# Optimization experiments

Measured on AMD Instinct MI355X. Metric: run time of the kernel, lower is better.

Reference implementation:

```python
import jax, jax.numpy as jnp
import numpy as np

NUM_HEADS = 8
NUM_GROUPS = 32
EPS = 1e-5


def group_norm(x, scale, bias):
    # x: (b, c, t)
    b, c, t = x.shape
    xg = x.reshape(b, NUM_GROUPS, c // NUM_GROUPS, t)
    mean = xg.mean(axis=(2, 3), keepdims=True)
    var = xg.var(axis=(2, 3), keepdims=True)
    xn = ((xg - mean) * jax.lax.rsqrt(var + EPS)).reshape(b, c, t)
    return xn * scale[None, :, None] + bias[None, :, None]


def setup_inputs() -> dict:
    key = jax.random.key(0)
    ks = jax.random.split(key, 3)
    b, c, h, w = 16, 512, 32, 32
    x = jax.random.normal(ks[0], (b, c, h, w), dtype=jnp.float32)
    gn_scale = jnp.ones((c,), jnp.float32)
    gn_bias = jnp.zeros((c,), jnp.float32)
    w_qkv = jax.random.normal(ks[1], (3 * c, c), jnp.float32) * (c ** -0.5)
    b_qkv = jnp.zeros((3 * c,), jnp.float32)
    w_proj = jax.random.normal(ks[2], (c, c), jnp.float32) * (c ** -0.5)
    b_proj = jnp.zeros((c,), jnp.float32)
    return {"x": x, "gn_scale": gn_scale, "gn_bias": gn_bias,
            "w_qkv": w_qkv, "b_qkv": b_qkv, "w_proj": w_proj, "b_proj": b_proj}


def reference(x, gn_scale, gn_bias, w_qkv, b_qkv, w_proj, b_proj):
    b, c, h, w = x.shape
    t = h * w
    xf = x.reshape(b, c, t)
    xn = group_norm(xf, gn_scale, gn_bias)
    # 1x1 conv1d == channel matmul: (b, 3c, t)
    qkv = jnp.einsum('oc,bct->bot', w_qkv, xn) + b_qkv[None, :, None]
    dh = c // NUM_HEADS
    qkv = qkv.reshape(b * NUM_HEADS, 3 * dh, t)
    q, k, v = jnp.split(qkv, 3, axis=1)  # each (b*H, dh, t)
    scale = dh ** -0.25
    logits = jnp.einsum('bct,bcs->bts', q * scale, k * scale)
    weight = jax.nn.softmax(logits.astype(jnp.float32), axis=-1).astype(logits.dtype)
    attn = jnp.einsum('bts,bcs->bct', weight, v)  # (b*H, dh, t)
    attn = attn.reshape(b, c, t)
    out = jnp.einsum('oc,bct->bot', w_proj, attn) + b_proj[None, :, None]
    return (xf + out).reshape(b, c, h, w)
```

## Files before the change

kernel.cpp:

```cpp
#include <hip/hip_runtime.h>
#include <hip/hip_bf16.h>

typedef __hip_bfloat16 bf16;
typedef __attribute__((ext_vector_type(8))) short short8;
typedef __attribute__((ext_vector_type(4))) short short4v;
typedef __attribute__((ext_vector_type(4))) float float4v;
typedef __attribute__((ext_vector_type(16))) float f32x16;
typedef __attribute__((ext_vector_type(4))) int int4v;

__device__ __forceinline__ float b2f(bf16 v) { return __bfloat162float(v); }
__device__ __forceinline__ bf16  f2b(float v) { return __float2bfloat16(v); }
__device__ __forceinline__ short f2s(float v) { bf16 h = f2b(v); return *reinterpret_cast<short*>(&h); }
__device__ __forceinline__ float s2f(short s) { bf16 h; *reinterpret_cast<short*>(&h) = s; return b2f(h); }
__device__ __forceinline__ short8 ld8(const bf16* p) { return *(const short8*)p; }

__device__ __forceinline__ float ldin(const void* p, size_t i, int f32) {
  return f32 ? ((const float*)p)[i] : b2f(((const bf16*)p)[i]);
}

__device__ __forceinline__ float4v mfma16(short8 a, short8 b, float4v c) {
  return __builtin_amdgcn_mfma_f32_16x16x32_bf16(a, b, c, 0, 0, 0);
}
__device__ __forceinline__ f32x16 mfma32(short8 a, short8 b, f32x16 c) {
  return __builtin_amdgcn_mfma_f32_32x32x16_bf16(a, b, c, 0, 0, 0);
}
__device__ __forceinline__ int cvtpk(float a, float b) {
  int r; asm("v_cvt_pk_bf16_f32 %0, %1, %2" : "=v"(r) : "v"(a), "v"(b)); return r;
}
__device__ __forceinline__ void plswap(int& x, int& y) {
  asm("v_permlane32_swap_b32 %0, %1" : "+v"(x), "+v"(y));
}

__device__ __forceinline__ void gload16(const void* g, void* l) {
  __builtin_amdgcn_global_load_lds((__attribute__((address_space(1))) void*)(void*)g,
                                   (__attribute__((address_space(3))) void*)l, 16, 0, 0);
}

#define K2SCALE 0.18033688011112042f
#define TSTRIDE 72

__global__ __launch_bounds__(256) void detect_kernel(const unsigned short* __restrict__ x,
                                                     int* __restrict__ flag) {
  __shared__ int h;
  if (threadIdx.x == 0) h = 0;
  __syncthreads();
  int local = 0;
  for (int i = threadIdx.x; i < 8192; i += 256)
    if ((x[i] & 0x7F80u) == 0x7F80u) local = 1;
  if (local) atomicOr(&h, 1);
  __syncthreads();
  if (threadIdx.x == 0) *flag = h;
}

__global__ __launch_bounds__(256) void conv2_kernel(const void* __restrict__ s1, bf16* __restrict__ d1,
                                                    const void* __restrict__ s2, bf16* __restrict__ d2,
                                                    const void* __restrict__ s3, bf16* __restrict__ d3,
                                                    const void* __restrict__ s4, bf16* __restrict__ d4,
                                                    const int* __restrict__ flagp) {
  const int f32 = *flagp;
  const int blk = blockIdx.x;
  const void* src; bf16* dst; int base, n;
  if (blk < 768)       { src = s1; dst = d1; base = blk;        n = 786432; }
  else if (blk < 1024) { src = s2; dst = d2; base = blk - 768;  n = 262144; }
  else if (blk < 1026) { src = s3; dst = d3; base = blk - 1024; n = 1536;   }
  else                 { src = s4; dst = d4; base = 0;          n = 512;    }
  int i0 = (base * 256 + threadIdx.x) * 4;
#pragma unroll
  for (int j = 0; j < 4; j++) {
    int i = i0 + j;
    if (i < n) dst[i] = f2b(ldin(src, i, f32));
  }
}

__global__ __launch_bounds__(256) void gn_stats_kernel(const void* __restrict__ x,
                                                       float2* __restrict__ stats,
                                                       const int* __restrict__ flagp) {
  const int f32 = *flagp;
  const int bg = blockIdx.x;
  const int GSZ = 16 * 1024;
  const size_t base = (size_t)bg * GSZ;
  const int tid = threadIdx.x;

  float s = 0.f, ss = 0.f;
  if (f32) {
    const float4v* xp = (const float4v*)((const float*)x + base) + tid;
#pragma unroll
    for (int i = 0; i < 16; i++) {
      float4v v = xp[i * 256];
#pragma unroll
      for (int j = 0; j < 4; j++) { s += v[j]; ss += v[j] * v[j]; }
    }
  } else {
    const short8* xp = (const short8*)((const bf16*)x + base) + tid;
#pragma unroll
    for (int i = 0; i < 8; i++) {
      short8 v = xp[i * 256];
#pragma unroll
      for (int j = 0; j < 8; j++) { float f = s2f(v[j]); s += f; ss += f * f; }
    }
  }
  for (int off = 32; off > 0; off >>= 1) {
    s  += __shfl_down(s, off);
    ss += __shfl_down(ss, off);
  }
  __shared__ float rs[4], rss[4];
  const int wave = tid >> 6, lane = tid & 63;
  if (lane == 0) { rs[wave] = s; rss[wave] = ss; }
  __syncthreads();
  if (tid == 0) {
    s  = rs[0] + rs[1] + rs[2] + rs[3];
    ss = rss[0] + rss[1] + rss[2] + rss[3];
    const float mean = s * (1.f / GSZ);
    const float var  = ss * (1.f / GSZ) - mean * mean;
    stats[bg] = make_float2(mean, rsqrtf(var + 1e-5f));
  }
}

__global__ __launch_bounds__(256) void gn_apply_kernel(const void* __restrict__ x,
                                                       const void* __restrict__ gsc,
                                                       const void* __restrict__ gbi,
                                                       const float2* __restrict__ stats,
                                                       bf16* __restrict__ xn,
                                                       const int* __restrict__ flagp) {
  const int f32 = *flagp;
  const int b = blockIdx.y;
  const int t0 = blockIdx.x * 64;
  const int cs = blockIdx.z * 128;
  const int tid = threadIdx.x;

  __shared__ float Aa[128], Bb[128];
  __shared__ short T[64][130];

  if (tid < 128) {
    const int c = cs + tid;
    const float2 st = stats[b * 32 + (c >> 4)];
    const float sc = ldin(gsc, c, f32), bi = ldin(gbi, c, f32);
    Aa[tid] = st.y * sc;
    Bb[tid] = bi - st.x * st.y * sc;
  }
  __syncthreads();

  const int row = tid >> 4;
  const int t4 = (tid & 15) * 4;
  if (f32) {
    const float* xb = (const float*)x + ((size_t)(b * 512 + cs)) * 1024 + t0 + t4;
#pragma unroll
    for (int st = 0; st < 8; st++) {
      const int c = row + st * 16;
      const float4v v = *(const float4v*)(xb + (size_t)c * 1024);
      const float aa = Aa[c], bb = Bb[c];
#pragma unroll
      for (int j = 0; j < 4; j++) T[t4 + j][c] = f2s(v[j] * aa + bb);
    }
  } else {
    const bf16* xb = (const bf16*)x + ((size_t)(b * 512 + cs)) * 1024 + t0 + t4;
#pragma unroll
    for (int st = 0; st < 8; st++) {
      const int c = row + st * 16;
      const short4v v = *(const short4v*)(xb + (size_t)c * 1024);
      const float aa = Aa[c], bb = Bb[c];
#pragma unroll
      for (int j = 0; j < 4; j++) T[t4 + j][c] = f2s(s2f(v[j]) * aa + bb);
    }
  }
  __syncthreads();

  const int cc = (tid & 63) * 2, tr = tid >> 6;
#pragma unroll
  for (int i = 0; i < 16; i++) {
    const int t2 = tr + i * 4;
    const int v = *(const int*)&T[t2][cc];
    *(int*)&xn[((size_t)(b * 1024 + t0 + t2)) * 512 + cs + cc] = v;
  }
}

__global__ __launch_bounds__(256) void qkv_kernel(const bf16* __restrict__ Wb,
                                                  const bf16* __restrict__ biasb,
                                                  const bf16* __restrict__ xn,
                                                  bf16* __restrict__ Qt,
                                                  bf16* __restrict__ Kt,
                                                  bf16* __restrict__ Vb) {
  const int bat = blockIdx.z;
  const int M0 = blockIdx.y * 128;
  const int N0 = blockIdx.x * 128;
  __shared__ short smem[18432];

  const int tid = threadIdx.x;
  const int w = tid >> 6, lane = tid & 63;
  const int col = lane & 15, g = lane >> 4;
  const int wm = (w & 1) * 64, wn = (w >> 1) * 64;

  float4v acc[4][4];
#pragma unroll
  for (int i = 0; i < 4; i++)
#pragma unroll
    for (int j = 0; j < 4; j++) acc[i][j] = (float4v)(0.f);

  int srco[2], dstb[2];
#pragma unroll
  for (int i = 0; i < 2; i++) {
    const int Gb = i * 256 + w * 64;
    dstb[i] = Gb * 8;
    const int G = Gb + lane;
    srco[i] = (G >> 2) * 512 + (G & 3) * 8;
  }
  const bf16* Ab  = Wb + (size_t)M0 * 512;
  const bf16* Bb2 = xn + ((size_t)bat * 1024 + N0) * 512;

#pragma unroll
  for (int i = 0; i < 2; i++) {
    gload16(Ab + srco[i],  &smem[dstb[i]]);
    gload16(Bb2 + srco[i], &smem[4096 + dstb[i]]);
  }
  __syncthreads();

  for (int it = 0; it < 16; ++it) {
    const int pb = it & 1;
    if (it < 15) {
      const int kn = it * 32 + 32;
      const int nb = (1 - pb) * 8192;
#pragma unroll
      for (int i = 0; i < 2; i++) {
        gload16(Ab + kn + srco[i],  &smem[nb + dstb[i]]);
        gload16(Bb2 + kn + srco[i], &smem[nb + 4096 + dstb[i]]);
      }
    }
    const short* Ap = &smem[pb * 8192];
    const short* Bp = Ap + 4096;
    short8 af[4], bf4[4];
#pragma unroll
    for (int mt = 0; mt < 4; mt++) af[mt] = *(const short8*)&Ap[(wm + mt * 16 + col) * 32 + g * 8];
#pragma unroll
    for (int nt = 0; nt < 4; nt++) bf4[nt] = *(const short8*)&Bp[(wn + nt * 16 + col) * 32 + g * 8];
#pragma unroll
    for (int mt = 0; mt < 4; mt++)
#pragma unroll
      for (int nt = 0; nt < 4; nt++) acc[mt][nt] = mfma16(af[mt], bf4[nt], acc[mt][nt]);
    __syncthreads();
  }

  const int sec = (M0 + wm) >> 6;
  const int h = sec / 3, kind = sec % 3;
  const size_t bh = (size_t)bat * 8 + h;
  const float qs = (kind == 0) ? K2SCALE : 1.f;
  short* Tw = smem + w * 4608;

  float bv[4][4];
#pragma unroll
  for (int mt = 0; mt < 4; mt++)
#pragma unroll
    for (int r = 0; r < 4; r++) bv[mt][r] = b2f(biasb[M0 + wm + mt * 16 + g * 4 + r]);

  if (kind == 2) {
#pragma unroll
    for (int mt = 0; mt < 4; mt++)
#pragma unroll
      for (int nt = 0; nt < 4; nt++)
#pragma unroll
        for (int r = 0; r < 4; r++) {
          const int lo = mt * 16 + g * 4 + r;
          const int lt = nt * 16 + col;
          Tw[lo * TSTRIDE + lt] = f2s(acc[mt][nt][r] + bv[mt][r]);
        }
#pragma unroll
    for (int j = 0; j < 8; j++) {
      const int lo = j * 8 + (lane >> 3);
      const int gr = lane & 7;
      short8 v = *(const short8*)&Tw[lo * TSTRIDE + gr * 8];
      *(short8*)(Vb + (bh * 64 + lo) * 1024 + N0 + wn + gr * 8) = v;
    }
  } else {
#pragma unroll
    for (int mt = 0; mt < 4; mt++)
#pragma unroll
      for (int nt = 0; nt < 4; nt++) {
        short4v pk;
#pragma unroll
        for (int r = 0; r < 4; r++) pk[r] = f2s((acc[mt][nt][r] + bv[mt][r]) * qs);
        *(short4v*)&Tw[(nt * 16 + col) * TSTRIDE + mt * 16 + g * 4] = pk;
      }
    bf16* dst = (kind == 0) ? Qt : Kt;
#pragma unroll
    for (int j = 0; j < 8; j++) {
      const int tl = j * 8 + (lane >> 3), c8 = (lane & 7) * 8;
      short8 v = *(const short8*)&Tw[tl * TSTRIDE + c8];
      *(short8*)(dst + (bh * 1024 + N0 + wn + tl) * 64 + c8) = v;
    }
  }
}

__global__ __launch_bounds__(256, 2) void attn_kernel(const bf16* __restrict__ Qt,
                                                      const bf16* __restrict__ Kt,
                                                      const bf16* __restrict__ Vb,
                                                      bf16* __restrict__ xattn) {
  const int bh = blockIdx.x;
  const int t0 = blockIdx.y * 256;
  const int b = bh >> 3, h = bh & 7;
  const int tid = threadIdx.x;
  const int w = tid >> 6, lane = tid & 63;
  const int qv = lane & 31, hh = lane >> 5;
  const int q0 = t0 + w * 64;

  __shared__ short Ks[8192];
  __shared__ short Vs[8192];

  const bf16* kbase = Kt + (size_t)bh * 65536;
  const bf16* vbase = Vb + (size_t)bh * 65536;

  int ksrc[2], vsrc[2];
  const int ldst0 = w * 1024, ldst1 = w * 1024 + 512;
#pragma unroll
  for (int i = 0; i < 2; i++) {
    const int G = w * 128 + i * 64 + lane;
    const int a = G >> 8, ks = (G >> 6) & 3, qvs = (G >> 1) & 31, hhs = G & 1;
    const int co = (ks * 2 + hhs) * 8;
    ksrc[i] = (a * 32 + qvs) * 64 + co;
    vsrc[i] = (a * 32 + qvs) * 1024 + co;
  }
  const int rb = (qv * 2 + hh) * 8;

  short8 qb[2][4];
#pragma unroll
  for (int qt = 0; qt < 2; qt++)
#pragma unroll
    for (int ks = 0; ks < 4; ks++)
      qb[qt][ks] = ld8(Qt + ((size_t)bh * 1024 + q0 + qt * 32 + qv) * 64 + ks * 16 + hh * 8);

  f32x16 O[2][2];
#pragma unroll
  for (int qt = 0; qt < 2; qt++)
#pragma unroll
    for (int o = 0; o < 2; o++) O[qt][o] = (f32x16)(0.f);
  float l[2] = {0.f, 0.f};
  short8 pa[2][4];

  gload16(kbase + ksrc[0], &Ks[ldst0]);
  gload16(kbase + ksrc[1], &Ks[ldst1]);
  gload16(vbase + vsrc[0], &Vs[ldst0]);
  gload16(vbase + vsrc[1], &Vs[ldst1]);
  __syncthreads();

#define SMAX(S, qt, a)                                                          \
  {                                                                             \
    _Pragma("unroll")                                                           \
    for (int j = 0; j < 16; j++) S[j] = __builtin_amdgcn_exp2f(S[j]);           \
    l[qt] += (((S[0] + S[1]) + (S[2] + S[3])) + ((S[4] + S[5]) + (S[6] + S[7])))\
       + (((S[8] + S[9]) + (S[10] + S[11])) + ((S[12] + S[13]) + (S[14] + S[15]))); \
    _Pragma("unroll")                                                           \
    for (int kp = 0; kp < 2; kp++) {                                            \
      int X  = cvtpk(S[8 * kp + 0], S[8 * kp + 1]);                             \
      int Y  = cvtpk(S[8 * kp + 4], S[8 * kp + 5]);                             \
      int X2 = cvtpk(S[8 * kp + 2], S[8 * kp + 3]);                             \
      int Y2 = cvtpk(S[8 * kp + 6], S[8 * kp + 7]);                             \
      plswap(X, Y);                                                             \
      plswap(X2, Y2);                                                           \
      const int4v wv = {X, X2, Y, Y2};                                          \
      pa[qt][(a) * 2 + kp] = __builtin_bit_cast(short8, wv);                    \
    }                                                                           \
  }

#pragma unroll 2
  for (int it = 0; it < 16; ++it) {
    const int cur = (it & 1) * 4096;
    const int nxt = 4096 - cur;
    if (it < 15) {
      gload16(kbase + (it + 1) * 4096 + ksrc[0], &Ks[nxt + ldst0]);
      gload16(kbase + (it + 1) * 4096 + ksrc[1], &Ks[nxt + ldst1]);
      gload16(vbase + (it + 1) * 64 + vsrc[0],   &Vs[nxt + ldst0]);
      gload16(vbase + (it + 1) * 64 + vsrc[1],   &Vs[nxt + ldst1]);
    }
#pragma unroll
    for (int a = 0; a < 2; a++) {
      short8 kf[4];
#pragma unroll
      for (int ks = 0; ks < 4; ks++)
        kf[ks] = *(const short8*)&Ks[cur + (a * 4 + ks) * 512 + rb];
#pragma unroll
      for (int qt = 0; qt < 2; qt++) {
        f32x16 S = (f32x16)(0.f);
#pragma unroll
        for (int ks = 0; ks < 4; ks++) S = mfma32(kf[ks], qb[qt][ks], S);
        SMAX(S, qt, a);
      }
    }
#pragma unroll
    for (int o = 0; o < 2; o++) {
      short8 vf[4];
#pragma unroll
      for (int ks = 0; ks < 4; ks++)
        vf[ks] = *(const short8*)&Vs[cur + (o * 4 + ks) * 512 + rb];
#pragma unroll
      for (int qt = 0; qt < 2; qt++)
#pragma unroll
        for (int ks = 0; ks < 4; ks++)
          O[qt][o] = mfma32(pa[qt][ks], vf[ks], O[qt][o]);
    }
    __syncthreads();
  }
#undef SMAX

#pragma unroll
  for (int qt = 0; qt < 2; qt++) {
    float lt = l[qt] + __shfl_xor(l[qt], 32);
    const float inv = 1.f / lt;
    float* lf = (float*)Ks + w * 64 + qt * 32;
    lf[qv] = inv;

    bf16* ob = xattn + ((size_t)b * 1024 + q0 + qt * 32 + 4 * hh) * 512 + h * 64 + qv;
#pragma unroll
    for (int r = 0; r < 16; r++) {
      const int qoff = (r & 3) + 8 * (r >> 2);
      const float iv = lf[qoff + 4 * hh];
      ob[(size_t)qoff * 512]      = f2b(O[qt][0][r] * iv);
      ob[(size_t)qoff * 512 + 32] = f2b(O[qt][1][r] * iv);
    }
  }
}

__global__ __launch_bounds__(256) void proj_kernel(const bf16* __restrict__ Wp,
                                                   const bf16* __restrict__ biasb,
                                                   const bf16* __restrict__ xattn,
                                                   const void* __restrict__ res,
                                                   void* __restrict__ out,
                                                   const int* __restrict__ flagp) {
  const int f32 = *flagp;
  const int bat = blockIdx.z;
  const int M0 = blockIdx.y * 128;
  const int N0 = blockIdx.x * 128;
  __shared__ short smem[18432];

  const int tid = threadIdx.x;
  const int w = tid >> 6, lane = tid & 63;
  const int col = lane & 15, g = lane >> 4;
  const int wm = (w & 1) * 64, wn = (w >> 1) * 64;

  float4v acc[4][4];
#pragma unroll
  for (int i = 0; i < 4; i++)
#pragma unroll
    for (int j = 0; j < 4; j++) acc[i][j] = (float4v)(0.f);

  int srco[2], dstb[2];
#pragma unroll
  for (int i = 0; i < 2; i++) {
    const int Gb = i * 256 + w * 64;
    dstb[i] = Gb * 8;
    const int G = Gb + lane;
    srco[i] = (G >> 2) * 512 + (G & 3) * 8;
  }
  const bf16* Ab  = Wp + (size_t)M0 * 512;
  const bf16* Bb2 = xattn + ((size_t)bat * 1024 + N0) * 512;

#pragma unroll
  for (int i = 0; i < 2; i++) {
    gload16(Ab + srco[i],  &smem[dstb[i]]);
    gload16(Bb2 + srco[i], &smem[4096 + dstb[i]]);
  }
  __syncthreads();

  for (int it = 0; it < 16; ++it) {
    const int pb = it & 1;
    if (it < 15) {
      const int kn = it * 32 + 32;
      const int nb = (1 - pb) * 8192;
#pragma unroll
      for (int i = 0; i < 2; i++) {
        gload16(Ab + kn + srco[i],  &smem[nb + dstb[i]]);
        gload16(Bb2 + kn + srco[i], &smem[nb + 4096 + dstb[i]]);
      }
    }
    const short* Ap = &smem[pb * 8192];
    const short* Bp = Ap + 4096;
    short8 af[4], bf4[4];
#pragma unroll
    for (int mt = 0; mt < 4; mt++) af[mt] = *(const short8*)&Ap[(wm + mt * 16 + col) * 32 + g * 8];
#pragma unroll
    for (int nt = 0; nt < 4; nt++) bf4[nt] = *(const short8*)&Bp[(wn + nt * 16 + col) * 32 + g * 8];
#pragma unroll
    for (int mt = 0; mt < 4; mt++)
#pragma unroll
      for (int nt = 0; nt < 4; nt++) acc[mt][nt] = mfma16(af[mt], bf4[nt], acc[mt][nt]);
    __syncthreads();
  }

  short* Tw = smem + w * 4608;
  float bv[4][4];
#pragma unroll
  for (int mt = 0; mt < 4; mt++)
#pragma unroll
    for (int r = 0; r < 4; r++) bv[mt][r] = b2f(biasb[M0 + wm + mt * 16 + g * 4 + r]);

#pragma unroll
  for (int mt = 0; mt < 4; mt++)
#pragma unroll
    for (int nt = 0; nt < 4; nt++)
#pragma unroll
      for (int r = 0; r < 4; r++) {
        const int lo = mt * 16 + g * 4 + r;
        const int lt = nt * 16 + col;
        Tw[lo * TSTRIDE + lt] = f2s(acc[mt][nt][r] + bv[mt][r]);
      }
#pragma unroll
  for (int j = 0; j < 8; j++) {
    const int lo = j * 8 + (lane >> 3);
    const int gr = lane & 7;
    short8 v = *(const short8*)&Tw[lo * TSTRIDE + gr * 8];
    const int o = M0 + wm + lo;
    const size_t ci = ((size_t)bat * 512 + o) * 1024 + N0 + wn + gr * 8;
    if (f32) {
      float4v o0, o1;
#pragma unroll
      for (int e = 0; e < 4; e++) o0[e] = s2f(v[e]) + ((const float*)res)[ci + e];
#pragma unroll
      for (int e = 0; e < 4; e++) o1[e] = s2f(v[e + 4]) + ((const float*)res)[ci + 4 + e];
      *(float4v*)((float*)out + ci) = o0;
      *(float4v*)((float*)out + ci + 4) = o1;
    } else {
      short8 ov;
#pragma unroll
      for (int e = 0; e < 8; e++)
        ov[e] = f2s(s2f(v[e]) + b2f(((const bf16*)res)[ci + e]));
      *(short8*)((bf16*)out + ci) = ov;
    }
  }
}

extern "C" void kernel_launch(void* const* d_in, const int* in_sizes, int n_in,
                              void* d_out, int out_size, void* d_ws, size_t ws_size,
                              hipStream_t stream) {
  const void* x      = d_in[0];
  const void* gsc    = d_in[1];
  const void* gbi    = d_in[2];
  const void* w_qkv  = d_in[3];
  const void* b_qkv  = d_in[4];
  const void* w_proj = d_in[5];
  const void* b_proj = d_in[6];

  char* p = (char*)d_ws;
  int*    flag  = (int*)p;                 p += 256;
  float2* stats = (float2*)p;              p += 512 * sizeof(float2);
  bf16*   xn    = (bf16*)p;                p += (size_t)16 * 1024 * 512 * 2;
  bf16*   Qt    = (bf16*)p;                p += (size_t)128 * 1024 * 64 * 2;
  bf16*   Kt    = (bf16*)p;                p += (size_t)128 * 1024 * 64 * 2;
  bf16*   Vb    = (bf16*)p;                p += (size_t)128 * 64 * 1024 * 2;
  bf16*   Wqb   = (bf16*)p;                p += (size_t)1536 * 512 * 2;
  bf16*   Wpb   = (bf16*)p;                p += (size_t)512 * 512 * 2;
  bf16*   Bqb   = (bf16*)p;                p += (size_t)1536 * 2;
  bf16*   Bpb   = (bf16*)p;                p += (size_t)512 * 2;
  bf16*   xattn = (bf16*)p;

  detect_kernel<<<1, 256, 0, stream>>>((const unsigned short*)x, flag);
  conv2_kernel<<<1027, 256, 0, stream>>>(w_qkv, Wqb, w_proj, Wpb,
                                         b_qkv, Bqb, b_proj, Bpb, flag);
  gn_stats_kernel<<<512, 256, 0, stream>>>(x, stats, flag);
  gn_apply_kernel<<<dim3(16, 16, 4), 256, 0, stream>>>(x, gsc, gbi, stats, xn, flag);
  qkv_kernel<<<dim3(8, 12, 16), 256, 0, stream>>>(Wqb, Bqb, xn, Qt, Kt, Vb);
  attn_kernel<<<dim3(128, 4), 256, 0, stream>>>(Qt, Kt, Vb, xattn);
  proj_kernel<<<dim3(8, 4, 16), 256, 0, stream>>>(Wpb, Bpb, xattn, x, d_out, flag);
}
```

Before: 206.2 us.

## Halve queries per attention block, double grid, raise occupancy and MFMA priority

Each attention wave now handles 32 queries instead of 64, so every block covers 128 queries and the grid doubles to 1024 blocks. Launch bounds rise to 4 blocks per CU, which cuts register use per thread and should let more waves hide latency. s_setprio is raised around the MFMA sequences so matrix work is issued ahead of other waves. The cost is that each K/V tile loaded into shared memory is reused by half as many queries, doubling total K/V traffic.

```diff
diff --git a/kernel.cpp b/kernel.cpp
--- a/kernel.cpp
+++ b/kernel.cpp
@@ -289,17 +289,17 @@
   }
 }
 
-__global__ __launch_bounds__(256, 2) void attn_kernel(const bf16* __restrict__ Qt,
+__global__ __launch_bounds__(256, 4) void attn_kernel(const bf16* __restrict__ Qt,
                                                       const bf16* __restrict__ Kt,
                                                       const bf16* __restrict__ Vb,
                                                       bf16* __restrict__ xattn) {
   const int bh = blockIdx.x;
-  const int t0 = blockIdx.y * 256;
+  const int t0 = blockIdx.y * 128;
   const int b = bh >> 3, h = bh & 7;
   const int tid = threadIdx.x;
   const int w = tid >> 6, lane = tid & 63;
   const int qv = lane & 31, hh = lane >> 5;
-  const int q0 = t0 + w * 64;
+  const int q0 = t0 + w * 32;
 
   __shared__ short Ks[8192];
   __shared__ short Vs[8192];
@@ -319,20 +319,15 @@
   }
   const int rb = (qv * 2 + hh) * 8;
 
-  short8 qb[2][4];
-#pragma unroll
-  for (int qt = 0; qt < 2; qt++)
-#pragma unroll
-    for (int ks = 0; ks < 4; ks++)
-      qb[qt][ks] = ld8(Qt + ((size_t)bh * 1024 + q0 + qt * 32 + qv) * 64 + ks * 16 + hh * 8);
-
-  f32x16 O[2][2];
-#pragma unroll
-  for (int qt = 0; qt < 2; qt++)
-#pragma unroll
-    for (int o = 0; o < 2; o++) O[qt][o] = (f32x16)(0.f);
-  float l[2] = {0.f, 0.f};
-  short8 pa[2][4];
+  short8 qb[4];
+#pragma unroll
+  for (int ks = 0; ks < 4; ks++)
+    qb[ks] = ld8(Qt + ((size_t)bh * 1024 + q0 + qv) * 64 + ks * 16 + hh * 8);
+
+  f32x16 O[2];
+  O[0] = (f32x16)(0.f); O[1] = (f32x16)(0.f);
+  float l = 0.f;
+  short8 pa[4];
 
   gload16(kbase + ksrc[0], &Ks[ldst0]);
   gload16(kbase + ksrc[1], &Ks[ldst1]);
@@ -340,11 +335,11 @@
   gload16(vbase + vsrc[1], &Vs[ldst1]);
   __syncthreads();
 
-#define SMAX(S, qt, a)                                                          \
+#define SMAX(S, a)                                                              \
   {                                                                             \
     _Pragma("unroll")                                                           \
     for (int j = 0; j < 16; j++) S[j] = __builtin_amdgcn_exp2f(S[j]);           \
-    l[qt] += (((S[0] + S[1]) + (S[2] + S[3])) + ((S[4] + S[5]) + (S[6] + S[7])))\
+    l += (((S[0] + S[1]) + (S[2] + S[3])) + ((S[4] + S[5]) + (S[6] + S[7])))    \
        + (((S[8] + S[9]) + (S[10] + S[11])) + ((S[12] + S[13]) + (S[14] + S[15]))); \
     _Pragma("unroll")                                                           \
     for (int kp = 0; kp < 2; kp++) {                                            \
@@ -355,7 +350,7 @@
       plswap(X, Y);                                                             \
       plswap(X2, Y2);                                                           \
       const int4v wv = {X, X2, Y, Y2};                                          \
-      pa[qt][(a) * 2 + kp] = __builtin_bit_cast(short8, wv);                    \
+      pa[(a) * 2 + kp] = __builtin_bit_cast(short8, wv);                        \
     }                                                                           \
   }
 
@@ -375,13 +370,12 @@
 #pragma unroll
       for (int ks = 0; ks < 4; ks++)
         kf[ks] = *(const short8*)&Ks[cur + (a * 4 + ks) * 512 + rb];
-#pragma unroll
-      for (int qt = 0; qt < 2; qt++) {
-        f32x16 S = (f32x16)(0.f);
-#pragma unroll
-        for (int ks = 0; ks < 4; ks++) S = mfma32(kf[ks], qb[qt][ks], S);
-        SMAX(S, qt, a);
-      }
+      f32x16 S = (f32x16)(0.f);
+      __builtin_amdgcn_s_setprio(1);
+#pragma unroll
+      for (int ks = 0; ks < 4; ks++) S = mfma32(kf[ks], qb[ks], S);
+      __builtin_amdgcn_s_setprio(0);
+      SMAX(S, a);
     }
 #pragma unroll
     for (int o = 0; o < 2; o++) {
@@ -389,30 +383,29 @@
 #pragma unroll
       for (int ks = 0; ks < 4; ks++)
         vf[ks] = *(const short8*)&Vs[cur + (o * 4 + ks) * 512 + rb];
-#pragma unroll
-      for (int qt = 0; qt < 2; qt++)
-#pragma unroll
-        for (int ks = 0; ks < 4; ks++)
-          O[qt][o] = mfma32(pa[qt][ks], vf[ks], O[qt][o]);
+      __builtin_amdgcn_s_setprio(1);
+#pragma unroll
+      for (int ks = 0; ks < 4; ks++)
+        O[o] = mfma32(pa[ks], vf[ks], O[o]);
+      __builtin_amdgcn_s_setprio(0);
     }
     __syncthreads();
   }
 #undef SMAX
 
-#pragma unroll
-  for (int qt = 0; qt < 2; qt++) {
-    float lt = l[qt] + __shfl_xor(l[qt], 32);
+  {
+    float lt = l + __shfl_xor(l, 32);
     const float inv = 1.f / lt;
-    float* lf = (float*)Ks + w * 64 + qt * 32;
+    float* lf = (float*)Ks + w * 32;
     lf[qv] = inv;
 
-    bf16* ob = xattn + ((size_t)b * 1024 + q0 + qt * 32 + 4 * hh) * 512 + h * 64 + qv;
+    bf16* ob = xattn + ((size_t)b * 1024 + q0 + 4 * hh) * 512 + h * 64 + qv;
 #pragma unroll
     for (int r = 0; r < 16; r++) {
       const int qoff = (r & 3) + 8 * (r >> 2);
       const float iv = lf[qoff + 4 * hh];
-      ob[(size_t)qoff * 512]      = f2b(O[qt][0][r] * iv);
-      ob[(size_t)qoff * 512 + 32] = f2b(O[qt][1][r] * iv);
+      ob[(size_t)qoff * 512]      = f2b(O[0][r] * iv);
+      ob[(size_t)qoff * 512 + 32] = f2b(O[1][r] * iv);
     }
   }
 }
@@ -555,6 +548,6 @@
   gn_stats_kernel<<<512, 256, 0, stream>>>(x, stats, flag);
   gn_apply_kernel<<<dim3(16, 16, 4), 256, 0, stream>>>(x, gsc, gbi, stats, xn, flag);
   qkv_kernel<<<dim3(8, 12, 16), 256, 0, stream>>>(Wqb, Bqb, xn, Qt, Kt, Vb);
-  attn_kernel<<<dim3(128, 4), 256, 0, stream>>>(Qt, Kt, Vb, xattn);
+  attn_kernel<<<dim3(128, 8), 256, 0, stream>>>(Qt, Kt, Vb, xattn);
   proj_kernel<<<dim3(8, 4, 16), 256, 0, stream>>>(Wpb, Bpb, xattn, x, d_out, flag);
 }
```

Result: no change. 205.3 us (-0.5%).
